# Performance work log

Measured on AMD Instinct MI355X. Metric: run time of the kernel, lower is better.

The kernel has to match this reference:

```python
import jax, jax.numpy as jnp
import numpy as np

B, C_LEN, Q_LEN, D = 8, 2048, 512, 1024


def setup_inputs() -> dict:
    key = jax.random.key(0)
    ks = jax.random.split(key, 10)
    scale = 1.0 / np.sqrt(D)
    return {
        "c": jax.random.normal(ks[0], (B, C_LEN, D), dtype=jnp.float32),
        "q": jax.random.normal(ks[1], (B, Q_LEN, D), dtype=jnp.float32),
        "w_cq": jax.random.normal(ks[2], (D,), dtype=jnp.float32) * scale,
        "b_cq": jax.random.normal(ks[3], (), dtype=jnp.float32) * scale,
        "w_c": jax.random.normal(ks[4], (D,), dtype=jnp.float32) * scale,
        "b_c": jax.random.normal(ks[5], (), dtype=jnp.float32) * scale,
        "w_q": jax.random.normal(ks[6], (D,), dtype=jnp.float32) * scale,
        "b_q": jax.random.normal(ks[7], (), dtype=jnp.float32) * scale,
        "W_l": jax.random.normal(ks[8], (D, 4 * D), dtype=jnp.float32) * (1.0 / np.sqrt(4 * D)),
        "b_l": jax.random.normal(ks[9], (D,), dtype=jnp.float32) * (1.0 / np.sqrt(4 * D)),
    }


def reference(c, q, w_cq, b_cq, w_c, b_c, w_q, b_q, W_l, b_l):
    # trilinear term: the original loops over q positions computing
    # att_weight_cq(c * q_i); since that Linear is rank-1, this is one einsum.
    cq = jnp.einsum('bcd,bqd,d->bcq', c, q, w_cq) + b_cq        # [B, C, Q]
    s = (c @ w_c + b_c)[:, :, None] + (q @ w_q + b_q)[:, None, :] + cq
    a = jax.nn.softmax(s, axis=2)                               # c2q attention
    c2q_att = jnp.einsum('bcq,bqd->bcd', a, q)                  # [B, C, D]
    b_att = jax.nn.softmax(jnp.max(s, axis=2), axis=1)          # [B, C]
    q2c_att = jnp.einsum('bc,bcd->bd', b_att, c)[:, None, :]    # [B, 1, D]
    x = jnp.concatenate([c, c2q_att, c * c2q_att, c * q2c_att], axis=-1)
    z = x @ W_l.T + b_l                                         # [B, C, D]
    return z
```

## Files before the change

### kernel.cpp

```cpp
#include <hip/hip_runtime.h>

typedef unsigned short u16;
typedef __attribute__((ext_vector_type(4))) float floatx4;
typedef __attribute__((ext_vector_type(4))) unsigned short u16x4;
typedef __attribute__((ext_vector_type(8))) short short8;
typedef __attribute__((ext_vector_type(8))) __bf16 bf16x8;

#define B_SZ 8
#define C_LEN 2048
#define Q_LEN 512
#define D_DIM 1024
#define K4 (4 * D_DIM)

static __device__ __forceinline__ u16 f2bf(float f) {
    union { float f; unsigned int u; } v; v.f = f;
    unsigned int r = v.u + 0x7FFFu + ((v.u >> 16) & 1u);
    return (u16)(r >> 16);
}
static __device__ __forceinline__ float bf2f(u16 h) {
    union { unsigned int u; float f; } v; v.u = ((unsigned int)h) << 16;
    return v.f;
}

static __device__ __forceinline__ void async16(const void* g, void* l) {
    __builtin_amdgcn_global_load_lds(
        (const __attribute__((address_space(1))) unsigned int*)g,
        (__attribute__((address_space(3))) unsigned int*)(unsigned int)(unsigned long long)l,
        16, 0, 0);
}

__global__ __launch_bounds__(256) void prep_kernel(
    const float* __restrict__ c, const float* __restrict__ q,
    const float* __restrict__ w_cq, const float* __restrict__ w_c, const float* __restrict__ w_q,
    u16* __restrict__ cbf, u16* __restrict__ qwbf, u16* __restrict__ qT,
    float* __restrict__ rowterm, float* __restrict__ colterm, float* __restrict__ q2c) {
    int blk = blockIdx.x;
    int tid = threadIdx.x;
    if (blk < 4096) {
        int row = blk * 4 + (tid >> 6);
        int lane = tid & 63;
        const float* src = c + (size_t)row * D_DIM;
        u16* dst = cbf + (size_t)row * D_DIM;
        float s = 0.f;
        #pragma unroll
        for (int j = 0; j < 4; ++j) {
            int idx = j * 256 + lane * 4;
            floatx4 a = *(const floatx4*)(src + idx);
            floatx4 w = *(const floatx4*)(w_c + idx);
            s += a[0]*w[0] + a[1]*w[1] + a[2]*w[2] + a[3]*w[3];
            u16x4 o;
            #pragma unroll
            for (int e = 0; e < 4; ++e) o[e] = f2bf(a[e]);
            *(u16x4*)(dst + idx) = o;
        }
        for (int off = 32; off; off >>= 1) s += __shfl_down(s, off);
        if (lane == 0) rowterm[row] = s;
    } else if (blk < 5120) {
        int row = (blk - 4096) * 4 + (tid >> 6);
        int lane = tid & 63;
        const float* src = q + (size_t)row * D_DIM;
        u16* dst = qwbf + (size_t)row * D_DIM;
        float s = 0.f;
        #pragma unroll
        for (int j = 0; j < 4; ++j) {
            int idx = j * 256 + lane * 4;
            floatx4 a  = *(const floatx4*)(src + idx);
            floatx4 wc = *(const floatx4*)(w_cq + idx);
            floatx4 wq = *(const floatx4*)(w_q + idx);
            s += a[0]*wq[0] + a[1]*wq[1] + a[2]*wq[2] + a[3]*wq[3];
            u16x4 o;
            #pragma unroll
            for (int e = 0; e < 4; ++e) o[e] = f2bf(a[e] * wc[e]);
            *(u16x4*)(dst + idx) = o;
        }
        for (int off = 32; off; off >>= 1) s += __shfl_down(s, off);
        if (lane == 0) colterm[row] = s;
    } else if (blk < 9216) {
        __shared__ float tile[32][33];
        int t = blk - 5120;
        int q0 = (t & 15) * 32;
        int d0 = ((t >> 4) & 31) * 32;
        int b = t >> 9;
        int tx = tid & 31, ty = tid >> 5;
        const float* qb = q + (size_t)b * Q_LEN * D_DIM;
        #pragma unroll
        for (int j = 0; j < 4; ++j) {
            int row = ty + j * 8;
            tile[row][tx] = qb[(size_t)(q0 + row) * D_DIM + d0 + tx];
        }
        __syncthreads();
        u16* qTb = qT + (size_t)b * D_DIM * Q_LEN;
        #pragma unroll
        for (int j = 0; j < 4; ++j) {
            int row = ty + j * 8;
            qTb[(size_t)(d0 + row) * Q_LEN + q0 + tx] = f2bf(tile[tx][row]);
        }
    } else {
        int i = (blk - 9216) * 256 + tid;
        q2c[i] = 0.0f;
    }
}

__global__ __launch_bounds__(256) void wmerge_all(const float* __restrict__ W, const float* __restrict__ q2c,
                                                  u16* __restrict__ Wm, u16* __restrict__ Wbf) {
    int n = blockIdx.x;
    int k = threadIdx.x * 4;
    const float* wr = W + (size_t)n * K4;
    floatx4 w1 = *(const floatx4*)(wr + k);
    floatx4 w4 = *(const floatx4*)(wr + 3072 + k);
    #pragma unroll
    for (int p = 0; p < 2; ++p) {
        int kk = p * 1024 + k;
        floatx4 v = *(const floatx4*)(wr + 1024 + kk);
        u16x4 o;
        #pragma unroll
        for (int e = 0; e < 4; ++e) o[e] = f2bf(v[e]);
        *(u16x4*)(Wbf + (size_t)n * 2048 + kk) = o;
    }
    #pragma unroll
    for (int b = 0; b < 8; ++b) {
        floatx4 g = *(const floatx4*)(q2c + (size_t)b * D_DIM + k);
        u16x4 o;
        #pragma unroll
        for (int e = 0; e < 4; ++e) o[e] = f2bf(w1[e] + w4[e] * g[e]);
        *(u16x4*)(Wm + (size_t)b * 1048576 + (size_t)n * 1024 + k) = o;
    }
}

template<int MODE>
__global__ __launch_bounds__(256) void gemm_async(
    const u16* __restrict__ A0, const u16* __restrict__ A1, const u16* __restrict__ A2,
    const u16* __restrict__ B0, const u16* __restrict__ B1, const u16* __restrict__ B2,
    const float* __restrict__ fB,
    float* __restrict__ of, u16* __restrict__ ob, const float* __restrict__ bias) {
    constexpr int NSEC = (MODE == 2) ? 3 : 1;
    constexpr int LDO  = (MODE == 0 || MODE == 3) ? 512 : 1024;
    constexpr int NTILES = (MODE == 0 || MODE == 3) ? 4 : 8;
    __shared__ u16 As[128 * 64];
    __shared__ u16 Bs[128 * 64];
    const int tid  = threadIdx.x;
    const int lane = tid & 63;
    const int wave = tid >> 6;
    const int lin  = blockIdx.x;
    const int b    = lin & 7;
    const int rem  = lin >> 3;
    const int n0   = (rem % NTILES) * 128;
    const int m0   = (rem / NTILES) * 128;

    const u16* Aarr[NSEC];
    const u16* Barr[NSEC];
    const float* Bf = nullptr;
    int lda_[NSEC], ldb_[NSEC], ks_[NSEC];
    if constexpr (MODE == 0) {
        Aarr[0] = A0 + (size_t)b * C_LEN * D_DIM; lda_[0] = 1024;
        Barr[0] = B0 + (size_t)b * Q_LEN * D_DIM; ldb_[0] = 1024; ks_[0] = 1024;
    } else if constexpr (MODE == 1) {
        Aarr[0] = A0 + (size_t)b * C_LEN * Q_LEN; lda_[0] = 512;
        Barr[0] = B0 + (size_t)b * D_DIM * Q_LEN; ldb_[0] = 512;  ks_[0] = 512;
    } else if constexpr (MODE == 3) {
        Aarr[0] = A0;                             lda_[0] = 2048;
        Barr[0] = nullptr;                        ldb_[0] = 1024;  ks_[0] = 1024;
        Bf = fB + (size_t)b * Q_LEN * D_DIM;
    } else {
        Aarr[0] = A0 + (size_t)b * C_LEN * D_DIM; lda_[0] = 1024;
        Barr[0] = B0 + (size_t)b * D_DIM * D_DIM; ldb_[0] = 1024;  ks_[0] = 1024;
        Aarr[1] = A1 + (size_t)b * C_LEN * Q_LEN; lda_[1] = 512;
        Barr[1] = B1 + (size_t)b * D_DIM * Q_LEN; ldb_[1] = 512;   ks_[1] = 512;
        Aarr[2] = A2 + (size_t)b * C_LEN * D_DIM; lda_[2] = 1024;
        Barr[2] = B2 + 1024;                      ldb_[2] = 2048;  ks_[2] = 1024;
    }

    const int srow = lane >> 3;
    const int ssc  = ((lane & 7) ^ srow) * 8;

    floatx4 acc[4][4];
    #pragma unroll
    for (int i = 0; i < 4; ++i)
        #pragma unroll
        for (int j = 0; j < 4; ++j)
            acc[i][j] = (floatx4)(0.0f);

    const int wrow = (wave >> 1) * 64;
    const int wcol = (wave & 1) * 64;
    const int quad = lane >> 4;
    const int lrow = lane & 15;
    const int sw7  = lane & 7;

    #pragma unroll
    for (int sec = 0; sec < NSEC; ++sec) {
        const u16* __restrict__ Ab = Aarr[sec];
        const u16* __restrict__ Bb = Barr[sec];
        const int LA = lda_[sec];
        const int LB = ldb_[sec];
        const int KS = ks_[sec];
        for (int k0 = 0; k0 < KS; k0 += 64) {
            #pragma unroll
            for (int cc = 0; cc < 4; ++cc) {
                int ch = wave * 4 + cc;
                int rr = ch * 8 + srow;
                async16(Ab + (size_t)(m0 + rr) * LA + k0 + ssc, &As[ch * 512]);
            }
            if constexpr (MODE == 3) {
                #pragma unroll
                for (int cc = 0; cc < 4; ++cc) {
                    int ch = wave * 4 + cc;
                    int rr = ch * 8 + srow;
                    const float* src = Bf + (size_t)(n0 + rr) * 1024 + k0 + ssc;
                    floatx4 v0 = *(const floatx4*)src;
                    floatx4 v1 = *(const floatx4*)(src + 4);
                    u16x4 o0, o1;
                    #pragma unroll
                    for (int e = 0; e < 4; ++e) { o0[e] = f2bf(v0[e]); o1[e] = f2bf(v1[e]); }
                    *(u16x4*)&Bs[ch * 512 + lane * 8]     = o0;
                    *(u16x4*)&Bs[ch * 512 + lane * 8 + 4] = o1;
                }
            } else {
                #pragma unroll
                for (int cc = 0; cc < 4; ++cc) {
                    int ch = wave * 4 + cc;
                    int rr = ch * 8 + srow;
                    async16(Bb + (size_t)(n0 + rr) * LB + k0 + ssc, &Bs[ch * 512]);
                }
            }
            __syncthreads();
            #pragma unroll
            for (int h = 0; h < 2; ++h) {
                const int pc = ((h * 4 + quad) ^ sw7) * 8;
                bf16x8 af[4], bfr[4];
                #pragma unroll
                for (int i = 0; i < 4; ++i)
                    af[i] = __builtin_bit_cast(bf16x8, *(const short8*)&As[(wrow + i*16 + lrow) * 64 + pc]);
                #pragma unroll
                for (int j = 0; j < 4; ++j)
                    bfr[j] = __builtin_bit_cast(bf16x8, *(const short8*)&Bs[(wcol + j*16 + lrow) * 64 + pc]);
                #pragma unroll
                for (int i = 0; i < 4; ++i)
                    #pragma unroll
                    for (int j = 0; j < 4; ++j)
                        acc[i][j] = __builtin_amdgcn_mfma_f32_16x16x32_bf16(af[i], bfr[j], acc[i][j], 0, 0, 0);
            }
            __syncthreads();
        }
    }

    float* ofb = nullptr; u16* obb = nullptr; const u16* cbr = nullptr;
    if (MODE == 0)      ofb = of + (size_t)b * C_LEN * Q_LEN;
    else if (MODE == 1) { obb = ob + (size_t)b * C_LEN * D_DIM; cbr = A1 + (size_t)b * C_LEN * D_DIM; }
    else if (MODE == 2) ofb = of + (size_t)b * C_LEN * D_DIM;
    else                obb = ob + (size_t)b * D_DIM * Q_LEN;
    #pragma unroll
    for (int i = 0; i < 4; ++i) {
        #pragma unroll
        for (int j = 0; j < 4; ++j) {
            #pragma unroll
            for (int e = 0; e < 4; ++e) {
                int gm = m0 + wrow + i * 16 + quad * 4 + e;
                int gn = n0 + wcol + j * 16 + lrow;
                float v = acc[i][j][e];
                if (MODE == 0)      ofb[(size_t)gm * LDO + gn] = v;
                else if (MODE == 1) {
                    float cv = bf2f(cbr[(size_t)gm * 1024 + gn]);
                    obb[(size_t)gm * LDO + gn] = f2bf(cv * v);
                }
                else if (MODE == 2) ofb[(size_t)gm * LDO + gn] = v + bias[gn];
                else                obb[(size_t)gm * LDO + gn] = f2bf(v);
            }
        }
    }
}

__global__ void softmax_kernel(const float* __restrict__ S, const float* __restrict__ colterm,
                               u16* __restrict__ P, float* __restrict__ mbuf) {
    int row = blockIdx.x * 4 + (threadIdx.x >> 6);
    int lane = threadIdx.x & 63;
    int b = row >> 11;
    const float* sp = S + (size_t)row * Q_LEN;
    const float* cp = colterm + (size_t)b * Q_LEN;
    float v[8];
    float m = -1e30f;
    #pragma unroll
    for (int j = 0; j < 8; ++j) {
        int idx = j * 64 + lane;
        v[j] = sp[idx] + cp[idx];
        m = fmaxf(m, v[j]);
    }
    for (int off = 32; off; off >>= 1) m = fmaxf(m, __shfl_xor(m, off));
    float s = 0.f;
    #pragma unroll
    for (int j = 0; j < 8; ++j) { v[j] = __expf(v[j] - m); s += v[j]; }
    for (int off = 32; off; off >>= 1) s += __shfl_xor(s, off);
    float inv = 1.0f / s;
    u16* pp = P + (size_t)row * Q_LEN;
    #pragma unroll
    for (int j = 0; j < 8; ++j) pp[j * 64 + lane] = f2bf(v[j] * inv);
    if (lane == 0) mbuf[row] = m;
}

__global__ __launch_bounds__(256) void batt_kernel(const float* __restrict__ mbuf,
                                                   const float* __restrict__ rowterm,
                                                   float* __restrict__ batt) {
    __shared__ float red[8];
    int b = blockIdx.x;
    int tid = threadIdx.x;
    const float* mb = mbuf + (size_t)b * C_LEN;
    const float* rt = rowterm + (size_t)b * C_LEN;
    float v[8];
    float m = -1e30f;
    #pragma unroll
    for (int j = 0; j < 8; ++j) { int idx = j * 256 + tid; v[j] = mb[idx] + rt[idx]; m = fmaxf(m, v[j]); }
    for (int off = 32; off; off >>= 1) m = fmaxf(m, __shfl_xor(m, off));
    int wave = tid >> 6, lane = tid & 63;
    if (lane == 0) red[wave] = m;
    __syncthreads();
    m = fmaxf(fmaxf(red[0], red[1]), fmaxf(red[2], red[3]));
    float s = 0.f;
    #pragma unroll
    for (int j = 0; j < 8; ++j) { v[j] = __expf(v[j] - m); s += v[j]; }
    for (int off = 32; off; off >>= 1) s += __shfl_xor(s, off);
    if (lane == 0) red[4 + wave] = s;
    __syncthreads();
    s = red[4] + red[5] + red[6] + red[7];
    float inv = 1.0f / s;
    float* bb = batt + (size_t)b * C_LEN;
    #pragma unroll
    for (int j = 0; j < 8; ++j) bb[j * 256 + tid] = v[j] * inv;
}

__global__ __launch_bounds__(256) void q2c_kernel(const float* __restrict__ batt,
                                                  const u16* __restrict__ cbf,
                                                  float* __restrict__ q2c) {
    int d  = blockIdx.x * 256 + threadIdx.x;
    int b  = blockIdx.y;
    int c0 = blockIdx.z * 256;
    const u16* cb = cbf + ((size_t)b * C_LEN + c0) * D_DIM + d;
    const float* bb = batt + (size_t)b * C_LEN + c0;
    float s = 0.f;
    #pragma unroll 4
    for (int i = 0; i < 256; ++i) s += bb[i] * bf2f(cb[(size_t)i * D_DIM]);
    atomicAdd(&q2c[(size_t)b * D_DIM + d], s);
}

extern "C" void kernel_launch(void* const* d_in, const int* in_sizes, int n_in,
                              void* d_out, int out_size, void* d_ws, size_t ws_size,
                              hipStream_t stream) {
    const float* c   = (const float*)d_in[0];
    const float* q   = (const float*)d_in[1];
    const float* wcq = (const float*)d_in[2];
    const float* w_c = (const float*)d_in[4];
    const float* w_q = (const float*)d_in[6];
    const float* W_l = (const float*)d_in[8];
    const float* b_l = (const float*)d_in[9];
    float* out = (float*)d_out;

    char* ws = (char*)d_ws;
    u16*   cbf     = (u16*)ws;
    float* S       = (float*)(ws + 33554432);
    u16*   cc2q    = (u16*)(ws + 33554432);
    u16*   qwbf    = (u16*)(ws + 67108864);
    u16*   W2q     = (u16*)(ws + 67108864);
    u16*   P       = (u16*)(ws + 75497472);
    u16*   qT      = (u16*)(ws + 92274688);
    u16*   Wm      = (u16*)(ws + 100663296);
    u16*   Wbf     = (u16*)(ws + 117440512);
    float* rowterm = (float*)(ws + 121634816);
    float* colterm = (float*)(ws + 121700352);
    float* mbuf    = (float*)(ws + 121716736);
    float* batt    = (float*)(ws + 121782272);
    float* q2c     = (float*)(ws + 121847808);

    prep_kernel<<<dim3(9248), dim3(256), 0, stream>>>(c, q, wcq, w_c, w_q,
                                                      cbf, qwbf, qT, rowterm, colterm, q2c);
    gemm_async<0><<<dim3(512), dim3(256), 0, stream>>>(cbf, nullptr, nullptr, qwbf, nullptr, nullptr,
                                                       nullptr, S, nullptr, nullptr);
    softmax_kernel<<<dim3(4096), dim3(256), 0, stream>>>(S, colterm, P, mbuf);
    batt_kernel<<<dim3(8), dim3(256), 0, stream>>>(mbuf, rowterm, batt);
    q2c_kernel<<<dim3(4, 8, 8), dim3(256), 0, stream>>>(batt, cbf, q2c);
    wmerge_all<<<dim3(1024), dim3(256), 0, stream>>>(W_l, q2c, Wm, Wbf);
    gemm_async<3><<<dim3(256), dim3(256), 0, stream>>>(Wbf, nullptr, nullptr, nullptr, nullptr, nullptr,
                                                       q, nullptr, W2q, nullptr);
    gemm_async<1><<<dim3(1024), dim3(256), 0, stream>>>(P, cbf, nullptr, qT, nullptr, nullptr,
                                                        nullptr, nullptr, cc2q, nullptr);
    gemm_async<2><<<dim3(1024), dim3(256), 0, stream>>>(cbf, P, cc2q, Wm, W2q, Wbf,
                                                        nullptr, out, nullptr, b_l);
}
```

Before: 365.9 us.

## Merge S and W2q GEMMs into one launch, fuse batt into q2c

The S = c·(q⊙w_cq) GEMM and the Wbf·q GEMM now run in a single launch of 768 blocks. q is loaded as fp32 and scaled by w_cq inside the GEMM B-tile load, so the separate qwbf buffer is gone. The Wbf bf16 conversion moves into the prep kernel, and the batt softmax is recomputed per block inside the q2c kernel, which removes two launches and the batt buffer. The cost is that every q2c block redundantly recomputes the batch softmax statistics, and the merged GEMM uses synchronous fp32 loads for its B tiles.

Measured after the change: 389.0 us. 1.06x slower.

```diff
diff --git a/kernel.cpp b/kernel.cpp
--- a/kernel.cpp
+++ b/kernel.cpp
@@ -31,8 +31,8 @@
 
 __global__ __launch_bounds__(256) void prep_kernel(
     const float* __restrict__ c, const float* __restrict__ q,
-    const float* __restrict__ w_cq, const float* __restrict__ w_c, const float* __restrict__ w_q,
-    u16* __restrict__ cbf, u16* __restrict__ qwbf, u16* __restrict__ qT,
+    const float* __restrict__ w_c, const float* __restrict__ w_q, const float* __restrict__ W,
+    u16* __restrict__ cbf, u16* __restrict__ qT, u16* __restrict__ Wbf,
     float* __restrict__ rowterm, float* __restrict__ colterm, float* __restrict__ q2c) {
     int blk = blockIdx.x;
     int tid = threadIdx.x;
@@ -59,19 +59,13 @@
         int row = (blk - 4096) * 4 + (tid >> 6);
         int lane = tid & 63;
         const float* src = q + (size_t)row * D_DIM;
-        u16* dst = qwbf + (size_t)row * D_DIM;
         float s = 0.f;
         #pragma unroll
         for (int j = 0; j < 4; ++j) {
             int idx = j * 256 + lane * 4;
             floatx4 a  = *(const floatx4*)(src + idx);
-            floatx4 wc = *(const floatx4*)(w_cq + idx);
             floatx4 wq = *(const floatx4*)(w_q + idx);
             s += a[0]*wq[0] + a[1]*wq[1] + a[2]*wq[2] + a[3]*wq[3];
-            u16x4 o;
-            #pragma unroll
-            for (int e = 0; e < 4; ++e) o[e] = f2bf(a[e] * wc[e]);
-            *(u16x4*)(dst + idx) = o;
         }
         for (int off = 32; off; off >>= 1) s += __shfl_down(s, off);
         if (lane == 0) colterm[row] = s;
@@ -95,28 +89,31 @@
             int row = ty + j * 8;
             qTb[(size_t)(d0 + row) * Q_LEN + q0 + tx] = f2bf(tile[tx][row]);
         }
+    } else if (blk < 10240) {
+        int n = blk - 9216;
+        const float* wr = W + (size_t)n * K4 + 1024;
+        #pragma unroll
+        for (int p = 0; p < 2; ++p) {
+            int kk = p * 1024 + tid * 4;
+            floatx4 v = *(const floatx4*)(wr + kk);
+            u16x4 o;
+            #pragma unroll
+            for (int e = 0; e < 4; ++e) o[e] = f2bf(v[e]);
+            *(u16x4*)(Wbf + (size_t)n * 2048 + kk) = o;
+        }
     } else {
-        int i = (blk - 9216) * 256 + tid;
+        int i = (blk - 10240) * 256 + tid;
         q2c[i] = 0.0f;
     }
 }
 
-__global__ __launch_bounds__(256) void wmerge_all(const float* __restrict__ W, const float* __restrict__ q2c,
-                                                  u16* __restrict__ Wm, u16* __restrict__ Wbf) {
+__global__ __launch_bounds__(256) void wmerge_Wm(const float* __restrict__ W, const float* __restrict__ q2c,
+                                                 u16* __restrict__ Wm) {
     int n = blockIdx.x;
     int k = threadIdx.x * 4;
     const float* wr = W + (size_t)n * K4;
     floatx4 w1 = *(const floatx4*)(wr + k);
     floatx4 w4 = *(const floatx4*)(wr + 3072 + k);
-    #pragma unroll
-    for (int p = 0; p < 2; ++p) {
-        int kk = p * 1024 + k;
-        floatx4 v = *(const floatx4*)(wr + 1024 + kk);
-        u16x4 o;
-        #pragma unroll
-        for (int e = 0; e < 4; ++e) o[e] = f2bf(v[e]);
-        *(u16x4*)(Wbf + (size_t)n * 2048 + kk) = o;
-    }
     #pragma unroll
     for (int b = 0; b < 8; ++b) {
         floatx4 g = *(const floatx4*)(q2c + (size_t)b * D_DIM + k);
@@ -134,40 +131,26 @@
     const float* __restrict__ fB,
     float* __restrict__ of, u16* __restrict__ ob, const float* __restrict__ bias) {
     constexpr int NSEC = (MODE == 2) ? 3 : 1;
-    constexpr int LDO  = (MODE == 0 || MODE == 3) ? 512 : 1024;
-    constexpr int NTILES = (MODE == 0 || MODE == 3) ? 4 : 8;
     __shared__ u16 As[128 * 64];
     __shared__ u16 Bs[128 * 64];
     const int tid  = threadIdx.x;
     const int lane = tid & 63;
     const int wave = tid >> 6;
     const int lin  = blockIdx.x;
-    const int b    = lin & 7;
-    const int rem  = lin >> 3;
-    const int n0   = (rem % NTILES) * 128;
-    const int m0   = (rem / NTILES) * 128;
-
-    const u16* Aarr[NSEC];
-    const u16* Barr[NSEC];
-    const float* Bf = nullptr;
-    int lda_[NSEC], ldb_[NSEC], ks_[NSEC];
-    if constexpr (MODE == 0) {
-        Aarr[0] = A0 + (size_t)b * C_LEN * D_DIM; lda_[0] = 1024;
-        Barr[0] = B0 + (size_t)b * Q_LEN * D_DIM; ldb_[0] = 1024; ks_[0] = 1024;
-    } else if constexpr (MODE == 1) {
-        Aarr[0] = A0 + (size_t)b * C_LEN * Q_LEN; lda_[0] = 512;
-        Barr[0] = B0 + (size_t)b * D_DIM * Q_LEN; ldb_[0] = 512;  ks_[0] = 512;
-    } else if constexpr (MODE == 3) {
-        Aarr[0] = A0;                             lda_[0] = 2048;
-        Barr[0] = nullptr;                        ldb_[0] = 1024;  ks_[0] = 1024;
-        Bf = fB + (size_t)b * Q_LEN * D_DIM;
+
+    int part = 0, b, rem, n0, m0;
+    if constexpr (MODE == 4) {
+        part = (lin >= 512) ? 1 : 0;
+        int t = part ? (lin - 512) : lin;
+        b   = t & 7;
+        rem = t >> 3;
+        n0  = (rem & 3) * 128;
+        m0  = (rem >> 2) * 128;
     } else {
-        Aarr[0] = A0 + (size_t)b * C_LEN * D_DIM; lda_[0] = 1024;
-        Barr[0] = B0 + (size_t)b * D_DIM * D_DIM; ldb_[0] = 1024;  ks_[0] = 1024;
-        Aarr[1] = A1 + (size_t)b * C_LEN * Q_LEN; lda_[1] = 512;
-        Barr[1] = B1 + (size_t)b * D_DIM * Q_LEN; ldb_[1] = 512;   ks_[1] = 512;
-        Aarr[2] = A2 + (size_t)b * C_LEN * D_DIM; lda_[2] = 1024;
-        Barr[2] = B2 + 1024;                      ldb_[2] = 2048;  ks_[2] = 1024;
+        b   = lin & 7;
+        rem = lin >> 3;
+        n0  = (rem & 7) * 128;
+        m0  = (rem >> 3) * 128;
     }
 
     const int srow = lane >> 3;
@@ -186,68 +169,107 @@
     const int lrow = lane & 15;
     const int sw7  = lane & 7;
 
-    #pragma unroll
-    for (int sec = 0; sec < NSEC; ++sec) {
-        const u16* __restrict__ Ab = Aarr[sec];
-        const u16* __restrict__ Bb = Barr[sec];
-        const int LA = lda_[sec];
-        const int LB = ldb_[sec];
-        const int KS = ks_[sec];
-        for (int k0 = 0; k0 < KS; k0 += 64) {
+    auto compute_tiles = [&]() {
+        #pragma unroll
+        for (int h = 0; h < 2; ++h) {
+            const int pc = ((h * 4 + quad) ^ sw7) * 8;
+            bf16x8 af[4], bfr[4];
+            #pragma unroll
+            for (int i = 0; i < 4; ++i)
+                af[i] = __builtin_bit_cast(bf16x8, *(const short8*)&As[(wrow + i*16 + lrow) * 64 + pc]);
+            #pragma unroll
+            for (int j = 0; j < 4; ++j)
+                bfr[j] = __builtin_bit_cast(bf16x8, *(const short8*)&Bs[(wcol + j*16 + lrow) * 64 + pc]);
+            #pragma unroll
+            for (int i = 0; i < 4; ++i)
+                #pragma unroll
+                for (int j = 0; j < 4; ++j)
+                    acc[i][j] = __builtin_amdgcn_mfma_f32_16x16x32_bf16(af[i], bfr[j], acc[i][j], 0, 0, 0);
+        }
+    };
+
+    if constexpr (MODE == 4) {
+        const u16* __restrict__ Ab = part ? A2 : (A0 + (size_t)b * C_LEN * D_DIM);
+        const int LA = part ? 2048 : 1024;
+        const float* __restrict__ Bfp = fB + (size_t)b * Q_LEN * D_DIM;
+        const bool wmul = (part == 0);
+        for (int k0 = 0; k0 < 1024; k0 += 64) {
             #pragma unroll
             for (int cc = 0; cc < 4; ++cc) {
                 int ch = wave * 4 + cc;
                 int rr = ch * 8 + srow;
                 async16(Ab + (size_t)(m0 + rr) * LA + k0 + ssc, &As[ch * 512]);
             }
-            if constexpr (MODE == 3) {
+            #pragma unroll
+            for (int cc = 0; cc < 4; ++cc) {
+                int ch = wave * 4 + cc;
+                int rr = ch * 8 + srow;
+                const float* src = Bfp + (size_t)(n0 + rr) * 1024 + k0 + ssc;
+                floatx4 v0 = *(const floatx4*)src;
+                floatx4 v1 = *(const floatx4*)(src + 4);
+                if (wmul) {
+                    floatx4 w0 = *(const floatx4*)(bias + k0 + ssc);
+                    floatx4 w1 = *(const floatx4*)(bias + k0 + ssc + 4);
+                    #pragma unroll
+                    for (int e = 0; e < 4; ++e) { v0[e] *= w0[e]; v1[e] *= w1[e]; }
+                }
+                u16x4 o0, o1;
+                #pragma unroll
+                for (int e = 0; e < 4; ++e) { o0[e] = f2bf(v0[e]); o1[e] = f2bf(v1[e]); }
+                *(u16x4*)&Bs[ch * 512 + lane * 8]     = o0;
+                *(u16x4*)&Bs[ch * 512 + lane * 8 + 4] = o1;
+            }
+            __syncthreads();
+            compute_tiles();
+            __syncthreads();
+        }
+    } else {
+        const u16* Aarr[NSEC];
+        const u16* Barr[NSEC];
+        int lda_[NSEC], ldb_[NSEC], ks_[NSEC];
+        if constexpr (MODE == 1) {
+            Aarr[0] = A0 + (size_t)b * C_LEN * Q_LEN; lda_[0] = 512;
+            Barr[0] = B0 + (size_t)b * D_DIM * Q_LEN; ldb_[0] = 512;  ks_[0] = 512;
+        } else {
+            Aarr[0] = A0 + (size_t)b * C_LEN * D_DIM; lda_[0] = 1024;
+            Barr[0] = B0 + (size_t)b * D_DIM * D_DIM; ldb_[0] = 1024;  ks_[0] = 1024;
+            Aarr[1] = A1 + (size_t)b * C_LEN * Q_LEN; lda_[1] = 512;
+            Barr[1] = B1 + (size_t)b * D_DIM * Q_LEN; ldb_[1] = 512;   ks_[1] = 512;
+            Aarr[2] = A2 + (size_t)b * C_LEN * D_DIM; lda_[2] = 1024;
+            Barr[2] = B2 + 1024;                      ldb_[2] = 2048;  ks_[2] = 1024;
+        }
+        #pragma unroll
+        for (int sec = 0; sec < NSEC; ++sec) {
+            const u16* __restrict__ Ab = Aarr[sec];
+            const u16* __restrict__ Bb = Barr[sec];
+            const int LA = lda_[sec];
+            const int LB = ldb_[sec];
+            const int KS = ks_[sec];
+            for (int k0 = 0; k0 < KS; k0 += 64) {
                 #pragma unroll
                 for (int cc = 0; cc < 4; ++cc) {
                     int ch = wave * 4 + cc;
                     int rr = ch * 8 + srow;
-                    const float* src = Bf + (size_t)(n0 + rr) * 1024 + k0 + ssc;
-                    floatx4 v0 = *(const floatx4*)src;
-                    floatx4 v1 = *(const floatx4*)(src + 4);
-                    u16x4 o0, o1;
-                    #pragma unroll
-                    for (int e = 0; e < 4; ++e) { o0[e] = f2bf(v0[e]); o1[e] = f2bf(v1[e]); }
-                    *(u16x4*)&Bs[ch * 512 + lane * 8]     = o0;
-                    *(u16x4*)&Bs[ch * 512 + lane * 8 + 4] = o1;
+                    async16(Ab + (size_t)(m0 + rr) * LA + k0 + ssc, &As[ch * 512]);
                 }
-            } else {
                 #pragma unroll
                 for (int cc = 0; cc < 4; ++cc) {
                     int ch = wave * 4 + cc;
                     int rr = ch * 8 + srow;
                     async16(Bb + (size_t)(n0 + rr) * LB + k0 + ssc, &Bs[ch * 512]);
                 }
+                __syncthreads();
+                compute_tiles();
+                __syncthreads();
             }
-            __syncthreads();
-            #pragma unroll
-            for (int h = 0; h < 2; ++h) {
-                const int pc = ((h * 4 + quad) ^ sw7) * 8;
-                bf16x8 af[4], bfr[4];
-                #pragma unroll
-                for (int i = 0; i < 4; ++i)
-                    af[i] = __builtin_bit_cast(bf16x8, *(const short8*)&As[(wrow + i*16 + lrow) * 64 + pc]);
-                #pragma unroll
-                for (int j = 0; j < 4; ++j)
-                    bfr[j] = __builtin_bit_cast(bf16x8, *(const short8*)&Bs[(wcol + j*16 + lrow) * 64 + pc]);
-                #pragma unroll
-                for (int i = 0; i < 4; ++i)
-                    #pragma unroll
-                    for (int j = 0; j < 4; ++j)
-                        acc[i][j] = __builtin_amdgcn_mfma_f32_16x16x32_bf16(af[i], bfr[j], acc[i][j], 0, 0, 0);
-            }
-            __syncthreads();
         }
     }
 
     float* ofb = nullptr; u16* obb = nullptr; const u16* cbr = nullptr;
-    if (MODE == 0)      ofb = of + (size_t)b * C_LEN * Q_LEN;
-    else if (MODE == 1) { obb = ob + (size_t)b * C_LEN * D_DIM; cbr = A1 + (size_t)b * C_LEN * D_DIM; }
-    else if (MODE == 2) ofb = of + (size_t)b * C_LEN * D_DIM;
-    else                obb = ob + (size_t)b * D_DIM * Q_LEN;
+    int ldo;
+    if constexpr (MODE == 1) { obb = ob + (size_t)b * C_LEN * D_DIM; cbr = A1 + (size_t)b * C_LEN * D_DIM; ldo = 1024; }
+    else if constexpr (MODE == 2) { ofb = of + (size_t)b * C_LEN * D_DIM; ldo = 1024; }
+    else { if (part == 0) ofb = of + (size_t)b * C_LEN * Q_LEN; else obb = ob + (size_t)b * D_DIM * Q_LEN; ldo = 512; }
     #pragma unroll
     for (int i = 0; i < 4; ++i) {
         #pragma unroll
@@ -257,13 +279,15 @@
                 int gm = m0 + wrow + i * 16 + quad * 4 + e;
                 int gn = n0 + wcol + j * 16 + lrow;
                 float v = acc[i][j][e];
-                if (MODE == 0)      ofb[(size_t)gm * LDO + gn] = v;
-                else if (MODE == 1) {
+                if constexpr (MODE == 1) {
                     float cv = bf2f(cbr[(size_t)gm * 1024 + gn]);
-                    obb[(size_t)gm * LDO + gn] = f2bf(cv * v);
+                    obb[(size_t)gm * ldo + gn] = f2bf(cv * v);
+                } else if constexpr (MODE == 2) {
+                    ofb[(size_t)gm * ldo + gn] = v + bias[gn];
+                } else {
+                    if (part == 0) ofb[(size_t)gm * ldo + gn] = v;
+                    else           obb[(size_t)gm * ldo + gn] = f2bf(v);
                 }
-                else if (MODE == 2) ofb[(size_t)gm * LDO + gn] = v + bias[gn];
-                else                obb[(size_t)gm * LDO + gn] = f2bf(v);
             }
         }
     }
@@ -296,12 +320,16 @@
     if (lane == 0) mbuf[row] = m;
 }
 
-__global__ __launch_bounds__(256) void batt_kernel(const float* __restrict__ mbuf,
-                                                   const float* __restrict__ rowterm,
-                                                   float* __restrict__ batt) {
+__global__ __launch_bounds__(256) void q2c_batt(const float* __restrict__ mbuf,
+                                                const float* __restrict__ rowterm,
+                                                const u16* __restrict__ cbf,
+                                                float* __restrict__ q2c) {
     __shared__ float red[8];
-    int b = blockIdx.x;
+    __shared__ float wlds[256];
     int tid = threadIdx.x;
+    int d  = blockIdx.x * 256 + tid;
+    int b  = blockIdx.y;
+    int cz = blockIdx.z;
     const float* mb = mbuf + (size_t)b * C_LEN;
     const float* rt = rowterm + (size_t)b * C_LEN;
     float v[8];
@@ -315,29 +343,18 @@
     m = fmaxf(fmaxf(red[0], red[1]), fmaxf(red[2], red[3]));
     float s = 0.f;
     #pragma unroll
-    for (int j = 0; j < 8; ++j) { v[j] = __expf(v[j] - m); s += v[j]; }
+    for (int j = 0; j < 8; ++j) s += __expf(v[j] - m);
     for (int off = 32; off; off >>= 1) s += __shfl_xor(s, off);
     if (lane == 0) red[4 + wave] = s;
     __syncthreads();
     s = red[4] + red[5] + red[6] + red[7];
-    float inv = 1.0f / s;
-    float* bb = batt + (size_t)b * C_LEN;
-    #pragma unroll
-    for (int j = 0; j < 8; ++j) bb[j * 256 + tid] = v[j] * inv;
-}
-
-__global__ __launch_bounds__(256) void q2c_kernel(const float* __restrict__ batt,
-                                                  const u16* __restrict__ cbf,
-                                                  float* __restrict__ q2c) {
-    int d  = blockIdx.x * 256 + threadIdx.x;
-    int b  = blockIdx.y;
-    int c0 = blockIdx.z * 256;
-    const u16* cb = cbf + ((size_t)b * C_LEN + c0) * D_DIM + d;
-    const float* bb = batt + (size_t)b * C_LEN + c0;
-    float s = 0.f;
+    wlds[tid] = __expf(v[cz] - m) / s;
+    __syncthreads();
+    const u16* cb = cbf + ((size_t)b * C_LEN + (size_t)cz * 256) * D_DIM + d;
+    float acc = 0.f;
     #pragma unroll 4
-    for (int i = 0; i < 256; ++i) s += bb[i] * bf2f(cb[(size_t)i * D_DIM]);
-    atomicAdd(&q2c[(size_t)b * D_DIM + d], s);
+    for (int i = 0; i < 256; ++i) acc += wlds[i] * bf2f(cb[(size_t)i * D_DIM]);
+    atomicAdd(&q2c[(size_t)b * D_DIM + d], acc);
 }
 
 extern "C" void kernel_launch(void* const* d_in, const int* in_sizes, int n_in,
@@ -356,7 +373,6 @@
     u16*   cbf     = (u16*)ws;
     float* S       = (float*)(ws + 33554432);
     u16*   cc2q    = (u16*)(ws + 33554432);
-    u16*   qwbf    = (u16*)(ws + 67108864);
     u16*   W2q     = (u16*)(ws + 67108864);
     u16*   P       = (u16*)(ws + 75497472);
     u16*   qT      = (u16*)(ws + 92274688);
@@ -365,19 +381,15 @@
     float* rowterm = (float*)(ws + 121634816);
     float* colterm = (float*)(ws + 121700352);
     float* mbuf    = (float*)(ws + 121716736);
-    float* batt    = (float*)(ws + 121782272);
-    float* q2c     = (float*)(ws + 121847808);
-
-    prep_kernel<<<dim3(9248), dim3(256), 0, stream>>>(c, q, wcq, w_c, w_q,
-                                                      cbf, qwbf, qT, rowterm, colterm, q2c);
-    gemm_async<0><<<dim3(512), dim3(256), 0, stream>>>(cbf, nullptr, nullptr, qwbf, nullptr, nullptr,
-                                                       nullptr, S, nullptr, nullptr);
+    float* q2c     = (float*)(ws + 121782272);
+
+    prep_kernel<<<dim3(10272), dim3(256), 0, stream>>>(c, q, w_c, w_q, W_l,
+                                                       cbf, qT, Wbf, rowterm, colterm, q2c);
+    gemm_async<4><<<dim3(768), dim3(256), 0, stream>>>(cbf, nullptr, Wbf, nullptr, nullptr, nullptr,
+                                                       q, S, W2q, wcq);
     softmax_kernel<<<dim3(4096), dim3(256), 0, stream>>>(S, colterm, P, mbuf);
-    batt_kernel<<<dim3(8), dim3(256), 0, stream>>>(mbuf, rowterm, batt);
-    q2c_kernel<<<dim3(4, 8, 8), dim3(256), 0, stream>>>(batt, cbf, q2c);
-    wmerge_all<<<dim3(1024), dim3(256), 0, stream>>>(W_l, q2c, Wm, Wbf);
-    gemm_async<3><<<dim3(256), dim3(256), 0, stream>>>(Wbf, nullptr, nullptr, nullptr, nullptr, nullptr,
-                                                       q, nullptr, W2q, nullptr);
+    q2c_batt<<<dim3(4, 8, 8), dim3(256), 0, stream>>>(mbuf, rowterm, cbf, q2c);
+    wmerge_Wm<<<dim3(1024), dim3(256), 0, stream>>>(W_l, q2c, Wm);
     gemm_async<1><<<dim3(1024), dim3(256), 0, stream>>>(P, cbf, nullptr, qT, nullptr, nullptr,
                                                         nullptr, nullptr, cc2q, nullptr);
     gemm_async<2><<<dim3(1024), dim3(256), 0, stream>>>(cbf, P, cc2q, Wm, W2q, Wbf,
```
